# Kernel tuning notes

Hardware: AMD Instinct MI355X
Metric: run time of the kernel (lower is better)

The kernel has to match this reference:

```python
import jax, jax.numpy as jnp
import numpy as np

N_HEADS = 8
ATT_DIM = 64


def _pos_enc(x):
    # x: (chan, L, bs, D); sinusoidal PE added along axis -3 (the query/key slot dim)
    L, D = x.shape[-3], x.shape[-1]
    pos = np.arange(L)[:, None].astype(np.float32)
    div = np.exp(np.arange(0, D, 2).astype(np.float32) * (-np.log(10000.0) / D))
    pe = np.zeros((L, 1, D), dtype=np.float32)
    pe[:, 0, 0::2] = np.sin(pos * div)
    pe[:, 0, 1::2] = np.cos(pos * div)
    return x + jnp.asarray(pe)


def setup_inputs() -> dict:
    key = jax.random.key(0)
    ks = jax.random.split(key, 6)
    C, NQ, NK, B, QD, KD = 8, 16, 32, 128, 128, 128
    E = N_HEADS * ATT_DIM  # 512
    OUT = ATT_DIM  # out_dim defaults to attention_dim
    b = np.float32(1.0 / np.sqrt(ATT_DIM))
    bp = np.float32(1.0 / np.sqrt(OUT))
    return {
        "q": jax.random.normal(ks[0], (C, NQ, B, QD), dtype=jnp.float32),
        "k": jax.random.normal(ks[1], (C, NK, B, KD), dtype=jnp.float32),
        "Wq": jax.random.uniform(ks[2], (C, NQ, QD, E), jnp.float32, -b, b),
        "Wk": jax.random.uniform(ks[3], (C, NK, KD, E), jnp.float32, -b, b),
        "Wv": jax.random.uniform(ks[4], (C, NK, KD, E), jnp.float32, -b, b),
        "Wp": jax.random.uniform(ks[5], (C, NQ, E, OUT), jnp.float32, -bp, bp),
    }


def reference(q, k, Wq, Wk, Wv, Wp):
    H, A = N_HEADS, ATT_DIM
    C, NQ, B, _ = q.shape
    NK = k.shape[1]
    inv_temp = jnp.float32(1.0 / np.sqrt(A))
    q_pe = _pos_enc(q)
    k_pe = _pos_enc(k)
    # per-channel grouped QKV projections: (C, N, B, D) x (C, N, D, E) -> (C, N, B, E)
    query = jnp.einsum('cqbd,cqde->cqbe', q_pe, Wq).reshape(C, NQ, B, H, A)
    key_t = jnp.einsum('ckbd,ckde->ckbe', k_pe, Wk).reshape(C, NK, B, H, A)
    value = jnp.einsum('ckbd,ckde->ckbe', k_pe, Wv).reshape(C, NK, B, H, A)
    # attention scores per (channel, batch, head)
    logits = jnp.einsum('cqbha,ckbha->cbhqk', query, key_t) * inv_temp
    attn = jax.nn.softmax(logits, axis=-1)
    # value aggregation (original does broadcast-multiply+sum; einsum is the same math)
    out = jnp.einsum('cbhqk,ckbha->cqbha', attn, value).reshape(C, NQ, B, H * A)
    # per-channel output projection
    return jnp.einsum('cqbe,cqeo->cqbo', out, Wp)
```

## Files before the change

kernel.cpp:

```cpp
#include <hip/hip_runtime.h>

#define C_  8
#define NQ_ 16
#define NK_ 32
#define B_  128
#define D_  128
#define E_  512
#define H_  8
#define A_  64
#define O_  64

typedef __attribute__((ext_vector_type(4))) float f32x4;
typedef __attribute__((ext_vector_type(8))) short bf16x8;
typedef __attribute__((ext_vector_type(4))) short bf16x4;

__device__ __forceinline__ short f2bf(float f) {
    union { float f; unsigned u; } v; v.f = f;
    unsigned r = v.u + 0x7fffu + ((v.u >> 16) & 1u);
    return (short)(r >> 16);
}

__global__ __launch_bounds__(256) void qkv_proj_kernel(
    const float* __restrict__ qin, const float* __restrict__ kin,
    const float* __restrict__ Wq, const float* __restrict__ Wk,
    const float* __restrict__ Wv,
    short* __restrict__ wsq, short* __restrict__ wsk, short* __restrict__ wsv)
{
    __shared__ __align__(16) short Alds[B_][72];
    __shared__ __align__(16) short Blds[128][72];
    __shared__ float pe_buf[D_];

    const int tid   = threadIdx.x;
    const int blk   = blockIdx.x;
    const int e_blk = blk & 3;
    const int unit  = blk >> 2;

    const float* X; const float* W; short* Y; int n; size_t ypitch;
    if (unit < C_ * NQ_) {
        const int c = unit >> 4;
        n = unit & 15;
        X = qin + (size_t)unit * B_ * D_;
        W = Wq  + (size_t)unit * D_ * E_;
        Y = wsq + (size_t)c * B_ * NQ_ * E_ + (size_t)n * E_;
        ypitch = (size_t)NQ_ * E_;
    } else if (unit < C_ * (NQ_ + NK_)) {
        const int u = unit - C_ * NQ_;
        const int c = u >> 5;
        n = u & 31;
        X = kin + (size_t)u * B_ * D_;
        W = Wk  + (size_t)u * D_ * E_;
        Y = wsk + (size_t)c * B_ * NK_ * E_ + (size_t)n * E_;
        ypitch = (size_t)NK_ * E_;
    } else {
        const int u = unit - C_ * (NQ_ + NK_);
        const int c = u >> 5;
        n = u & 31;
        X = kin + (size_t)u * B_ * D_;
        W = Wv  + (size_t)u * D_ * E_;
        Y = wsv + (size_t)c * B_ * NK_ * E_ + (size_t)n * E_;
        ypitch = (size_t)NK_ * E_;
    }

    if (tid < D_) {
        const int d = tid;
        const float freq = expf((float)(d & ~1) * (-9.210340371976184f / (float)D_));
        const float arg  = (float)n * freq;
        pe_buf[d] = (d & 1) ? cosf(arg) : sinf(arg);
    }
    __syncthreads();

    const int wv   = tid >> 6;
    const int lane = tid & 63;
    const int lr   = lane & 15;
    const int quad = lane >> 4;
    const int wrow = (wv >> 1) * 64;
    const int wcol = (wv & 1) * 64;

    f32x4 acc[4][4];
    for (int m = 0; m < 4; ++m)
        for (int nf = 0; nf < 4; ++nf)
            acc[m][nf] = (f32x4){0.f, 0.f, 0.f, 0.f};

    const int e  = tid & 127;
    const int kg = (tid >> 7) * 32;

    for (int k0 = 0; k0 < D_; k0 += 64) {
        f32x4 a_raw[8];
        #pragma unroll
        for (int i = 0; i < 8; ++i) {
            const int id  = tid + 256 * i;
            const int row = id >> 4;
            const int ch  = id & 15;
            a_raw[i] = *(const f32x4*)(X + (size_t)row * D_ + k0 + ch * 4);
        }
        float b_raw[32];
        const float* bsrc = W + (size_t)(k0 + kg) * E_ + e_blk * 128 + e;
        #pragma unroll
        for (int i = 0; i < 32; ++i)
            b_raw[i] = bsrc[(size_t)i * E_];

        #pragma unroll
        for (int i = 0; i < 8; ++i) {
            const int id  = tid + 256 * i;
            const int row = id >> 4;
            const int ch  = id & 15;
            bf16x4 v;
            #pragma unroll
            for (int j = 0; j < 4; ++j)
                v[j] = f2bf(a_raw[i][j] + pe_buf[k0 + ch * 4 + j]);
            *(bf16x4*)&Alds[row][ch * 4] = v;
        }
        #pragma unroll
        for (int i = 0; i < 4; ++i) {
            bf16x8 v;
            #pragma unroll
            for (int j = 0; j < 8; ++j)
                v[j] = f2bf(b_raw[i * 8 + j]);
            *(bf16x8*)&Blds[e][kg + i * 8] = v;
        }
        __syncthreads();

        for (int ks = 0; ks < 2; ++ks) {
            const int kc = ks * 32 + quad * 8;
            bf16x8 af[4], bfr[4];
            for (int m = 0; m < 4; ++m)
                af[m] = *(const bf16x8*)&Alds[wrow + m * 16 + lr][kc];
            for (int nf = 0; nf < 4; ++nf)
                bfr[nf] = *(const bf16x8*)&Blds[wcol + nf * 16 + lr][kc];
            for (int m = 0; m < 4; ++m)
                for (int nf = 0; nf < 4; ++nf)
                    acc[m][nf] = __builtin_amdgcn_mfma_f32_16x16x32_bf16(
                        af[m], bfr[nf], acc[m][nf], 0, 0, 0);
        }
        __syncthreads();
    }

    for (int m = 0; m < 4; ++m)
        for (int nf = 0; nf < 4; ++nf)
            for (int r = 0; r < 4; ++r) {
                const int row = wrow + m * 16 + quad * 4 + r;
                const int col = e_blk * 128 + wcol + nf * 16 + lr;
                Y[(size_t)row * ypitch + col] = f2bf(acc[m][nf][r]);
            }
}

__global__ __launch_bounds__(256) void attn_kernel(
    const short* __restrict__ wsq, const short* __restrict__ wsk,
    const short* __restrict__ wsv, short* __restrict__ wso)
{
    __shared__ __align__(16) short Ks[32][264];
    __shared__ __align__(16) short Vs[32][258];
    __shared__ __align__(16) short Ps[4][16][40];

    const int tid = threadIdx.x;
    const int pb  = blockIdx.x;
    const int b   = pb & (B_ - 1);
    const int c   = pb >> 7;

    const short* qb0 = wsq + ((size_t)(c * B_ + b) * NQ_) * E_;
    const short* kb0 = wsk + ((size_t)(c * B_ + b) * NK_) * E_;
    const short* vb0 = wsv + ((size_t)(c * B_ + b) * NK_) * E_;
    short*       ob0 = wso + ((size_t)(c * NQ_) * B_ + b) * E_;

    const int wv   = tid >> 6;
    const int lane = tid & 63;
    const int lr   = lane & 15;
    const int quad = lane >> 4;
    const int lcol = wv * 64;
    const int nloc = tid >> 5;
    const int ch   = tid & 31;

    auto loadKV = [&](const short* kb, const short* vb,
                      bf16x8 (&kr)[4], bf16x8 (&vr)[4]) {
        #pragma unroll
        for (int i = 0; i < 4; ++i)
            kr[i] = *(const bf16x8*)(kb + (size_t)(nloc + i * 8) * E_ + ch * 8);
        #pragma unroll
        for (int i = 0; i < 4; ++i)
            vr[i] = *(const bf16x8*)(vb + (size_t)(nloc + i * 8) * E_ + ch * 8);
    };
    auto writeKV = [&](bf16x8 (&kr)[4], bf16x8 (&vr)[4]) {
        #pragma unroll
        for (int i = 0; i < 4; ++i)
            *(bf16x8*)&Ks[nloc + i * 8][ch * 8] = kr[i];
        #pragma unroll
        for (int i = 0; i < 4; ++i)
            #pragma unroll
            for (int p = 0; p < 4; ++p)
                *(int*)&Vs[nloc + i * 8][ch * 8 + p * 2] = ((const int*)&vr[i])[p];
    };

    auto computeUnit = [&](const short* qb, short* ob) {
        const bf16x8 aq0 = *(const bf16x8*)(qb + (size_t)lr * E_ + lcol + quad * 8);
        const bf16x8 aq1 = *(const bf16x8*)(qb + (size_t)lr * E_ + lcol + 32 + quad * 8);

        f32x4 sacc0 = (f32x4){0.f, 0.f, 0.f, 0.f};
        f32x4 sacc1 = (f32x4){0.f, 0.f, 0.f, 0.f};
        {
            const int kc0 = lcol + quad * 8;
            sacc0 = __builtin_amdgcn_mfma_f32_16x16x32_bf16(aq0, *(const bf16x8*)&Ks[lr][kc0], sacc0, 0, 0, 0);
            sacc1 = __builtin_amdgcn_mfma_f32_16x16x32_bf16(aq0, *(const bf16x8*)&Ks[16 + lr][kc0], sacc1, 0, 0, 0);
            const int kc1 = lcol + 32 + quad * 8;
            sacc0 = __builtin_amdgcn_mfma_f32_16x16x32_bf16(aq1, *(const bf16x8*)&Ks[lr][kc1], sacc0, 0, 0, 0);
            sacc1 = __builtin_amdgcn_mfma_f32_16x16x32_bf16(aq1, *(const bf16x8*)&Ks[16 + lr][kc1], sacc1, 0, 0, 0);
        }

        float p0[4], p1[4];
        #pragma unroll
        for (int r = 0; r < 4; ++r) {
            const float v0 = sacc0[r] * 0.125f;
            const float v1 = sacc1[r] * 0.125f;
            float m = fmaxf(v0, v1);
            m = fmaxf(m, __shfl_xor(m, 1));
            m = fmaxf(m, __shfl_xor(m, 2));
            m = fmaxf(m, __shfl_xor(m, 4));
            m = fmaxf(m, __shfl_xor(m, 8));
            const float e0 = __expf(v0 - m);
            const float e1 = __expf(v1 - m);
            float s = e0 + e1;
            s += __shfl_xor(s, 1);
            s += __shfl_xor(s, 2);
            s += __shfl_xor(s, 4);
            s += __shfl_xor(s, 8);
            const float inv = 1.0f / s;
            p0[r] = e0 * inv;
            p1[r] = e1 * inv;
        }

        #pragma unroll
        for (int r = 0; r < 4; ++r) {
            Ps[wv][quad * 4 + r][lr]      = f2bf(p0[r]);
            Ps[wv][quad * 4 + r][16 + lr] = f2bf(p1[r]);
        }
        __syncthreads();
        const bf16x8 ap = *(const bf16x8*)&Ps[wv][lr][quad * 8];

        short* Osb = ((short*)Ks) + wv * 1024;

        #pragma unroll
        for (int t = 0; t < 4; ++t) {
            bf16x8 bvv;
            #pragma unroll
            for (int j = 0; j < 8; ++j)
                bvv[j] = Vs[quad * 8 + j][lcol + t * 16 + lr];
            f32x4 oacc = (f32x4){0.f, 0.f, 0.f, 0.f};
            oacc = __builtin_amdgcn_mfma_f32_16x16x32_bf16(ap, bvv, oacc, 0, 0, 0);
            #pragma unroll
            for (int r = 0; r < 4; ++r)
                Osb[(quad * 4 + r) * 64 + t * 16 + lr] = f2bf(oacc[r]);
        }

        const int q   = lane >> 2;
        const int seg = lane & 3;
        const bf16x8 oA = *(const bf16x8*)&Osb[q * 64 + seg * 16];
        const bf16x8 oB = *(const bf16x8*)&Osb[q * 64 + seg * 16 + 8];
        short* dst = ob + (size_t)q * (B_ * E_) + lcol + seg * 16;
        *(bf16x8*)dst       = oA;
        *(bf16x8*)(dst + 8) = oB;
    };

    bf16x8 kr0[4], vr0[4], kr1[4], vr1[4];
    loadKV(kb0, vb0, kr0, vr0);
    writeKV(kr0, vr0);
    __syncthreads();

    loadKV(kb0 + 256, vb0 + 256, kr1, vr1);
    computeUnit(qb0, ob0);
    __syncthreads();

    writeKV(kr1, vr1);
    __syncthreads();
    computeUnit(qb0 + 256, ob0 + 256);
}

__global__ __launch_bounds__(256) void out_proj_kernel(
    const short* __restrict__ wso, const float* __restrict__ Wp,
    float* __restrict__ out)
{
    __shared__ __align__(16) short Xlds[32 * 512];
    __shared__ __align__(16) short Wlds[32 * 512];

    const int tid = threadIdx.x;
    const int blk = blockIdx.x;
    const int cq  = blk >> 3;
    const int bh  = (blk >> 1) & 3;
    const int oh  = blk & 1;

    const short* Xb = wso + (size_t)cq * B_ * E_ + (size_t)bh * 32 * E_;
    const float* Wb = Wp  + (size_t)cq * E_ * O_ + oh * 32;
    float*       Ob = out + (size_t)cq * B_ * O_ + (size_t)bh * 32 * O_ + oh * 32;

    const int xrow = tid >> 3;
    const int xch  = tid & 7;
    const int o    = tid & 31;
    const int kg   = tid >> 5;

    bf16x8 xv[8];
    #pragma unroll
    for (int s = 0; s < 8; ++s)
        xv[s] = *(const bf16x8*)(Xb + (size_t)xrow * E_ + s * 64 + xch * 8);

    float wr[8][8];
    #pragma unroll
    for (int s = 0; s < 8; ++s)
        #pragma unroll
        for (int j = 0; j < 8; ++j)
            wr[s][j] = Wb[(size_t)(s * 64 + kg * 8 + j) * O_ + o];

    #pragma unroll
    for (int s = 0; s < 8; ++s) {
        const int g = (s * 8 + xch) ^ (xrow & 7);
        *(bf16x8*)&Xlds[xrow * 512 + g * 8] = xv[s];
    }
    #pragma unroll
    for (int s = 0; s < 8; ++s) {
        bf16x8 w8;
        #pragma unroll
        for (int j = 0; j < 8; ++j) w8[j] = f2bf(wr[s][j]);
        const int g = (s * 8 + kg) ^ (o & 7);
        *(bf16x8*)&Wlds[o * 512 + g * 8] = w8;
    }
    __syncthreads();

    const int wv   = tid >> 6;
    const int lane = tid & 63;
    const int lr   = lane & 15;
    const int quad = lane >> 4;
    const int rowh = wv >> 1;
    const int ohh  = wv & 1;
    const int arow = rowh * 16 + lr;
    const int brow = ohh * 16 + lr;

    f32x4 acc = (f32x4){0.f, 0.f, 0.f, 0.f};
    #pragma unroll
    for (int st = 0; st < 16; ++st) {
        const int ga = (st * 4 + quad) ^ (arow & 7);
        const int gb = (st * 4 + quad) ^ (brow & 7);
        const bf16x8 af  = *(const bf16x8*)&Xlds[arow * 512 + ga * 8];
        const bf16x8 bfr = *(const bf16x8*)&Wlds[brow * 512 + gb * 8];
        acc = __builtin_amdgcn_mfma_f32_16x16x32_bf16(af, bfr, acc, 0, 0, 0);
    }

    #pragma unroll
    for (int r = 0; r < 4; ++r)
        Ob[(size_t)(rowh * 16 + quad * 4 + r) * O_ + ohh * 16 + lr] = acc[r];
}

extern "C" void kernel_launch(void* const* d_in, const int* in_sizes, int n_in,
                              void* d_out, int out_size, void* d_ws, size_t ws_size,
                              hipStream_t stream) {
    const float* q  = (const float*)d_in[0];
    const float* k  = (const float*)d_in[1];
    const float* Wq = (const float*)d_in[2];
    const float* Wk = (const float*)d_in[3];
    const float* Wv = (const float*)d_in[4];
    const float* Wp = (const float*)d_in[5];
    float* out = (float*)d_out;

    const size_t sz_q = (size_t)C_ * NQ_ * B_ * E_;
    const size_t sz_k = (size_t)C_ * NK_ * B_ * E_;
    short* wsq = (short*)d_ws;
    short* wsk = wsq + sz_q;
    short* wsv = wsk + sz_k;
    short* wso = wsv + sz_k;

    qkv_proj_kernel<<<dim3(2560), dim3(256), 0, stream>>>(q, k, Wq, Wk, Wv, wsq, wsk, wsv);
    attn_kernel<<<dim3(1024), dim3(256), 0, stream>>>(wsq, wsk, wsv, wso);
    out_proj_kernel<<<dim3(1024), dim3(256), 0, stream>>>(wso, Wp, out);
}
```

Before: 252.4 us.

## Load QKV projection MFMA fragments directly from global, dropping LDS staging

New measurement: 269.9 us. 6.9% more time.

```diff
diff --git a/kernel.cpp b/kernel.cpp
--- a/kernel.cpp
+++ b/kernel.cpp
@@ -26,10 +26,6 @@
     const float* __restrict__ Wv,
     short* __restrict__ wsq, short* __restrict__ wsk, short* __restrict__ wsv)
 {
-    __shared__ __align__(16) short Alds[B_][72];
-    __shared__ __align__(16) short Blds[128][72];
-    __shared__ float pe_buf[D_];
-
     const int tid   = threadIdx.x;
     const int blk   = blockIdx.x;
     const int e_blk = blk & 3;
@@ -61,82 +57,86 @@
         ypitch = (size_t)NK_ * E_;
     }
 
-    if (tid < D_) {
-        const int d = tid;
-        const float freq = expf((float)(d & ~1) * (-9.210340371976184f / (float)D_));
-        const float arg  = (float)n * freq;
-        pe_buf[d] = (d & 1) ? cosf(arg) : sinf(arg);
-    }
-    __syncthreads();
-
     const int wv   = tid >> 6;
     const int lane = tid & 63;
     const int lr   = lane & 15;
     const int quad = lane >> 4;
     const int wrow = (wv >> 1) * 64;
     const int wcol = (wv & 1) * 64;
+    const int ecol = e_blk * 128 + wcol;
 
     f32x4 acc[4][4];
+    #pragma unroll
     for (int m = 0; m < 4; ++m)
+        #pragma unroll
         for (int nf = 0; nf < 4; ++nf)
             acc[m][nf] = (f32x4){0.f, 0.f, 0.f, 0.f};
 
-    const int e  = tid & 127;
-    const int kg = (tid >> 7) * 32;
-
+    #pragma unroll
     for (int k0 = 0; k0 < D_; k0 += 64) {
-        f32x4 a_raw[8];
-        #pragma unroll
-        for (int i = 0; i < 8; ++i) {
-            const int id  = tid + 256 * i;
-            const int row = id >> 4;
-            const int ch  = id & 15;
-            a_raw[i] = *(const f32x4*)(X + (size_t)row * D_ + k0 + ch * 4);
-        }
-        float b_raw[32];
-        const float* bsrc = W + (size_t)(k0 + kg) * E_ + e_blk * 128 + e;
-        #pragma unroll
-        for (int i = 0; i < 32; ++i)
-            b_raw[i] = bsrc[(size_t)i * E_];
-
-        #pragma unroll
-        for (int i = 0; i < 8; ++i) {
-            const int id  = tid + 256 * i;
-            const int row = id >> 4;
-            const int ch  = id & 15;
-            bf16x4 v;
-            #pragma unroll
-            for (int j = 0; j < 4; ++j)
-                v[j] = f2bf(a_raw[i][j] + pe_buf[k0 + ch * 4 + j]);
-            *(bf16x4*)&Alds[row][ch * 4] = v;
-        }
-        #pragma unroll
-        for (int i = 0; i < 4; ++i) {
-            bf16x8 v;
+        float peval;
+        {
+            const int d = k0 + lane;
+            const float freq = expf((float)(d & ~1) * (-9.210340371976184f / (float)D_));
+            const float arg  = (float)n * freq;
+            peval = (d & 1) ? cosf(arg) : sinf(arg);
+        }
+
+        #pragma unroll
+        for (int ks = 0; ks < 2; ++ks) {
+            const int kc = k0 + ks * 32 + quad * 8;
+
+            f32x4 a0[4], a1[4];
+            #pragma unroll
+            for (int m = 0; m < 4; ++m) {
+                const float* ar = X + (size_t)(wrow + m * 16 + lr) * D_ + kc;
+                a0[m] = *(const f32x4*)ar;
+                a1[m] = *(const f32x4*)(ar + 4);
+            }
+
+            float bw[4][8];
+            #pragma unroll
+            for (int nf = 0; nf < 4; ++nf) {
+                const float* br = W + (size_t)kc * E_ + ecol + nf * 16 + lr;
+                #pragma unroll
+                for (int j = 0; j < 8; ++j)
+                    bw[nf][j] = br[(size_t)j * E_];
+            }
+
+            float pj[8];
             #pragma unroll
             for (int j = 0; j < 8; ++j)
-                v[j] = f2bf(b_raw[i * 8 + j]);
-            *(bf16x8*)&Blds[e][kg + i * 8] = v;
-        }
-        __syncthreads();
-
-        for (int ks = 0; ks < 2; ++ks) {
-            const int kc = ks * 32 + quad * 8;
+                pj[j] = __shfl(peval, ks * 32 + quad * 8 + j);
+
             bf16x8 af[4], bfr[4];
+            #pragma unroll
+            for (int m = 0; m < 4; ++m) {
+                #pragma unroll
+                for (int j = 0; j < 4; ++j) {
+                    af[m][j]     = f2bf(a0[m][j] + pj[j]);
+                    af[m][4 + j] = f2bf(a1[m][j] + pj[4 + j]);
+                }
+            }
+            #pragma unroll
+            for (int nf = 0; nf < 4; ++nf)
+                #pragma unroll
+                for (int j = 0; j < 8; ++j)
+                    bfr[nf][j] = f2bf(bw[nf][j]);
+
+            #pragma unroll
             for (int m = 0; m < 4; ++m)
-                af[m] = *(const bf16x8*)&Alds[wrow + m * 16 + lr][kc];
-            for (int nf = 0; nf < 4; ++nf)
-                bfr[nf] = *(const bf16x8*)&Blds[wcol + nf * 16 + lr][kc];
-            for (int m = 0; m < 4; ++m)
+                #pragma unroll
                 for (int nf = 0; nf < 4; ++nf)
                     acc[m][nf] = __builtin_amdgcn_mfma_f32_16x16x32_bf16(
                         af[m], bfr[nf], acc[m][nf], 0, 0, 0);
         }
-        __syncthreads();
-    }
-
+    }
+
+    #pragma unroll
     for (int m = 0; m < 4; ++m)
+        #pragma unroll
         for (int nf = 0; nf < 4; ++nf)
+            #pragma unroll
             for (int r = 0; r < 4; ++r) {
                 const int row = wrow + m * 16 + quad * 4 + r;
                 const int col = e_blk * 128 + wcol + nf * 16 + lr;
```
